# Kernel optimization log

Hardware: AMD Instinct MI355X
Metric: run time of the kernel (lower is better)

## Reference

```python
import jax, jax.numpy as jnp
import numpy as np
import math

NLAT, NLON = 46, 90      # equiangular grid (in_shape == out_shape)
CH = 256                 # channels == kdim == vdim
BATCH = 1

def _cc_weights(n):
    # Clenshaw-Curtis quadrature weights (Waldvogel), nodes cos(k*pi/(n-1)); matches torch-harmonics equiangular grid
    n1 = n - 1
    N = np.arange(1, n1, 2)
    l = len(N)
    m = n1 - l
    v = np.concatenate([2.0 / N / (N - 2), [1.0 / N[-1]], np.zeros(m)])
    v = -v[:-1] - v[-1:0:-1]
    g0 = -np.ones(n1)
    g0[l] += n1
    g0[m] += n1
    g = g0 / (n1 ** 2 - 1 + (n1 % 2))
    w = np.fft.ifft(v + g).real
    return np.concatenate([w, w[:1]])

def _precompute_sparsity():
    # replicates _precompute_neighborhood_sparsity_s2: YZY-rotated north pole indicator within theta_cutoff
    lats = np.linspace(0.0, math.pi, NLAT)               # colatitudes of equiangular grid
    quad = (2.0 * math.pi / NLON) * _cc_weights(NLAT)    # per-latitude quadrature weights
    cutoff = math.pi / (NLAT - 1)                        # default theta_cutoff
    lons = np.linspace(0.0, 2.0 * math.pi, NLON + 1)[:-1]
    rows, cols = [], []
    for t in range(NLAT):
        a = -lats[t]
        beta = lons[None, :]
        gamma = lats[:, None]
        z = -np.cos(beta) * np.sin(a) * np.sin(gamma) + np.cos(a) * np.cos(gamma)
        x = np.cos(a) * np.cos(beta) * np.sin(gamma) + np.cos(gamma) * np.sin(a)
        y = np.sin(beta) * np.sin(gamma)
        nrm = np.sqrt(x * x + y * y + z * z)
        theta = np.arccos(np.clip(z / nrm, -1.0, 1.0))
        ii, jj = np.nonzero(theta <= cutoff)
        rows.append(np.full(ii.shape, t, dtype=np.int64))
        cols.append(ii * NLON + jj)
    row_ids = np.concatenate(rows).astype(np.int32)   # CSR row id per nnz (sorted)
    col_idx = np.concatenate(cols).astype(np.int32)   # flattened input index (at wo=0)
    return row_ids, col_idx, quad.astype(np.float32)

def setup_inputs() -> dict:
    key = jax.random.key(0)
    ks = jax.random.split(key, 9)
    row_ids, col_idx, quad = _precompute_sparsity()
    scale = 0.02  # sane init scale (module uses raw randn; trained weights would be O(this))
    return {
        "qo": jax.random.normal(ks[0], (BATCH, CH, NLAT, NLON), dtype=jnp.float32),
        "ki": jax.random.normal(ks[1], (BATCH, CH, NLAT, NLON), dtype=jnp.float32),
        "vi": jax.random.normal(ks[2], (BATCH, CH, NLAT, NLON), dtype=jnp.float32),
        "q_w": jax.random.normal(ks[3], (CH, CH), dtype=jnp.float32) * scale,
        "k_w": jax.random.normal(ks[4], (CH, CH), dtype=jnp.float32) * scale,
        "v_w": jax.random.normal(ks[5], (CH, CH), dtype=jnp.float32) * scale,
        "q_b": jax.random.normal(ks[6], (CH,), dtype=jnp.float32) * scale,
        "k_b": jax.random.normal(ks[7], (CH,), dtype=jnp.float32) * scale,
        "v_b": jax.random.normal(ks[8], (CH,), dtype=jnp.float32) * scale,
        "quad_w": jnp.asarray(quad),
        "row_ids": jnp.asarray(row_ids),
        "col_idx": jnp.asarray(col_idx),
    }

def reference(qo, ki, vi, q_w, k_w, v_w, q_b, k_b, v_b, quad_w, row_ids, col_idx):
    nlat, nlon = qo.shape[2], qo.shape[3]
    # 1x1 conv projections (F.conv2d with [out,in,1,1] kernels)
    q = jnp.einsum("kc,bchw->bkhw", q_w, qo) + q_b[None, :, None, None]
    k = jnp.einsum("kc,bchw->bkhw", k_w, ki) + k_b[None, :, None, None]
    v = jnp.einsum("vc,bchw->bvhw", v_w, vi) + v_b[None, :, None, None]

    hi = col_idx // nlon                                   # [N] input latitude per nnz
    wi0 = col_idx % nlon                                   # [N] input longitude at wo=0
    wo = jnp.arange(nlon)
    wi = (wi0[:, None] + wo[None, :]) % nlon               # [N, nlon] longitudes rotated by output lon

    kg = k[:, :, hi[:, None], wi]                          # [B, kdim, N, nlon] gathered keys
    qg = q[:, :, row_ids, :]                               # [B, kdim, N, nlon] query of owning output row
    qdotk = jnp.einsum("bcnw,bcnw->nbw", qg, kg)           # [N, B, nlon]

    # quadrature-weighted softmax over each output point's neighborhood (segment = output latitude row)
    seg_max = jax.ops.segment_max(qdotk, row_ids, num_segments=nlat, indices_are_sorted=True)
    seg_max = jax.lax.stop_gradient(seg_max)               # max shift cancels exactly in the ratio
    alpha = jnp.exp(qdotk - seg_max[row_ids]) * quad_w[hi][:, None, None]   # [N, B, nlon]
    denom = jax.ops.segment_sum(alpha, row_ids, num_segments=nlat, indices_are_sorted=True)  # [nlat, B, nlon]

    vg = jnp.transpose(v[:, :, hi[:, None], wi], (2, 0, 1, 3))   # [N, B, vdim, nlon]
    num = jax.ops.segment_sum(alpha[:, :, None, :] * vg, row_ids, num_segments=nlat, indices_are_sorted=True)
    out = num / denom[:, :, None, :]                       # [nlat, B, vdim, nlon]
    return jnp.transpose(out, (1, 2, 0, 3))                # [B, vdim, nlat, nlon]
```

## Files before the change

kernel.cpp:

```cpp
#include <hip/hip_runtime.h>
#include <math.h>

#define NLAT 46
#define NLON 90
#define CH   256
#define HW   (NLAT*NLON)
#define HWP  4160
#define HWT  64
#define NHT  65
#define XSTR 264

#define HEAVY_PER_XCD 45
#define LIGHT_GROUPS_PER_ROW 23
#define LIGHT_UNITS   (42*LIGHT_GROUPS_PER_ROW)
#define LIGHT_PER_XCD 121
#define SLOTS_PER_XCD (HEAVY_PER_XCD + LIGHT_PER_XCD)

typedef __attribute__((ext_vector_type(8))) short short8;
typedef __attribute__((ext_vector_type(4))) float floatx4;

__device__ __forceinline__ ushort f2bf(float f){
  uint u = __float_as_uint(f);
  u += 0x7fff + ((u >> 16) & 1);
  return (ushort)(u >> 16);
}
__device__ __forceinline__ float bf2fs(short s){
  return __uint_as_float(((uint)(ushort)s) << 16);
}

__device__ __forceinline__ int lower_bound_i(const int* __restrict__ a, int n, int key){
  int lo = 0, hi = n;
  while (lo < hi){ int mid = (lo + hi) >> 1; if (a[mid] < key) lo = mid + 1; else hi = mid; }
  return lo;
}

__global__ __launch_bounds__(256) void fproj_kernel(
    const float* __restrict__ qo, const float* __restrict__ ki, const float* __restrict__ vi,
    const float* __restrict__ qw, const float* __restrict__ kw, const float* __restrict__ vw,
    const float* __restrict__ qb, const float* __restrict__ kb, const float* __restrict__ vb,
    ushort* __restrict__ qP, ushort* __restrict__ kP, ushort* __restrict__ vP)
{
  const float* X; const float* Wf; const float* Bias; ushort* Out;
  if (blockIdx.y == 0){ X = qo; Wf = qw; Bias = qb; Out = qP; }
  else if (blockIdx.y == 1){ X = ki; Wf = kw; Bias = kb; Out = kP; }
  else { X = vi; Wf = vw; Bias = vb; Out = vP; }

  __shared__ ushort Xs[HWT][XSTR];

  const int tid = threadIdx.x;
  const int hw0 = blockIdx.x * HWT;

  {
    int hwL = tid & 63;
    int cb  = tid >> 6;
    int hw  = hw0 + hwL;
    bool ok = hw < HW;
    const float* Xp = X + (size_t)(cb*64)*HW + (ok ? hw : 0);
    #pragma unroll
    for (int gq = 0; gq < 8; gq++){
      short8 pk;
      #pragma unroll
      for (int u = 0; u < 8; u++){
        float f = ok ? Xp[(size_t)(gq*8 + u)*HW] : 0.f;
        pk[u] = (short)f2bf(f);
      }
      *(short8*)(&Xs[hwL][cb*64 + gq*8]) = pk;
    }
  }
  __syncthreads();

  const int lane = tid & 63;
  const int wave = tid >> 6;
  const int lm = lane & 15;
  const int lq = lane >> 4;
  const int kout_w = wave * 64;

  const float* Apf = Wf + (size_t)(kout_w + lm)*CH + lq*8;

  floatx4 acc[4][4];
  #pragma unroll
  for (int i = 0; i < 4; i++)
    #pragma unroll
    for (int j = 0; j < 4; j++) acc[i][j] = (floatx4){0,0,0,0};

  #pragma unroll
  for (int k0 = 0; k0 < 8; k0++){
    short8 a[4], b[4];
    #pragma unroll
    for (int i = 0; i < 4; i++){
      const float* p = Apf + (size_t)i*16*CH + k0*32;
      float4 w0 = *(const float4*)p;
      float4 w1 = *(const float4*)(p + 4);
      a[i][0] = (short)f2bf(w0.x); a[i][1] = (short)f2bf(w0.y);
      a[i][2] = (short)f2bf(w0.z); a[i][3] = (short)f2bf(w0.w);
      a[i][4] = (short)f2bf(w1.x); a[i][5] = (short)f2bf(w1.y);
      a[i][6] = (short)f2bf(w1.z); a[i][7] = (short)f2bf(w1.w);
    }
    #pragma unroll
    for (int j = 0; j < 4; j++)
      b[j] = *(const short8*)(&Xs[j*16 + lm][lq*8 + k0*32]);
    #pragma unroll
    for (int i = 0; i < 4; i++)
      #pragma unroll
      for (int j = 0; j < 4; j++)
        acc[i][j] = __builtin_amdgcn_mfma_f32_16x16x32_bf16(a[i], b[j], acc[i][j], 0, 0, 0);
  }

  #pragma unroll
  for (int i = 0; i < 4; i++){
    int kout = kout_w + i*16 + lq*4;
    float4 bias = *(const float4*)(Bias + kout);
    #pragma unroll
    for (int j = 0; j < 4; j++){
      int hw = hw0 + j*16 + lm;
      if (hw < HW){
        ushort4 o;
        o.x = f2bf(acc[i][j][0] + bias.x);
        o.y = f2bf(acc[i][j][1] + bias.y);
        o.z = f2bf(acc[i][j][2] + bias.z);
        o.w = f2bf(acc[i][j][3] + bias.w);
        *(ushort4*)(Out + (size_t)hw*CH + kout) = o;
      }
    }
  }
}

__device__ __forceinline__ void load_q16(const ushort* __restrict__ qP, int row, int gl, float* qf){
  const ushort* qrow = qP + (size_t)row * CH + gl*16;
  short8 q0 = *(const short8*)(qrow);
  short8 q1 = *(const short8*)(qrow + 8);
  #pragma unroll
  for (int u = 0; u < 8; u++){ qf[u] = bf2fs(q0[u]); qf[8+u] = bf2fs(q1[u]); }
}

__device__ __forceinline__ void visit(
    const ushort* __restrict__ kP, const ushort* __restrict__ vP,
    const uint* s_p, const float* s_qw,
    int n, int wo, int gl, const float* qf, float& den, float* acc)
{
  uint p  = s_p[n];
  int base = (int)(p & 0xffffu);
  int wi0  = (int)(p >> 16);
  int adj  = base + wo - ((wi0 + wo >= NLON) ? NLON : 0);
  size_t off = (size_t)adj * CH + gl*16;
  const short8* kp8 = (const short8*)(kP + off);
  short8 k0 = kp8[0], k1 = kp8[1];
  float s = 0.f;
  #pragma unroll
  for (int u = 0; u < 8; u++){
    s += qf[u]   * bf2fs(k0[u]);
    s += qf[8+u] * bf2fs(k1[u]);
  }
  s += __shfl_xor(s, 1, 64);
  s += __shfl_xor(s, 2, 64);
  s += __shfl_xor(s, 4, 64);
  s += __shfl_xor(s, 8, 64);
  float e = __expf(s) * s_qw[n];
  const short8* vp8 = (const short8*)(vP + off);
  short8 v0 = vp8[0], v1 = vp8[1];
  den += e;
  #pragma unroll
  for (int u = 0; u < 8; u++){
    acc[u]   += e * bf2fs(v0[u]);
    acc[8+u] += e * bf2fs(v1[u]);
  }
}

__global__ __launch_bounds__(256) void attn_kernel(
    const ushort* __restrict__ qP, const ushort* __restrict__ kP, const ushort* __restrict__ vP,
    const float* __restrict__ quad_w, const int* __restrict__ row_ids,
    const int* __restrict__ col_idx, int nnz, float* __restrict__ out)
{
  const int bid  = blockIdx.x;
  const int xcd  = bid & 7;
  const int slot = bid >> 3;

  int t, wo0, heavy;
  if (slot < HEAVY_PER_XCD){
    heavy = 1;
    int hu   = xcd * HEAVY_PER_XCD + slot;
    int hidx = hu / NLON;
    t   = (hidx < 2) ? hidx : 42 + hidx;
    wo0 = hu - hidx * NLON;
  } else {
    heavy = 0;
    int lu = xcd * LIGHT_PER_XCD + (slot - HEAVY_PER_XCD);
    if (lu >= LIGHT_UNITS) return;
    int li = lu / LIGHT_GROUPS_PER_ROW;
    t   = li + 2;
    wo0 = (lu - li * LIGHT_GROUPS_PER_ROW) * 4;
  }

  const int tid  = threadIdx.x;
  const int lane = tid & 63;
  const int wave = tid >> 6;
  const int g    = lane >> 4;
  const int gl   = lane & 15;

  const int start = lower_bound_i(row_ids, nnz, t);
  const int end   = lower_bound_i(row_ids, nnz, t + 1);
  const int nv    = end - start;

  __shared__ uint  s_p[256];
  __shared__ float s_qw[256];
  __shared__ float sden[4];
  __shared__ float sacc[4][CH];

  for (int n = tid; n < nv; n += 256){
    int ci  = col_idx[start + n];
    int hi  = ci / NLON;
    int wi0 = ci - hi * NLON;
    s_p[n]  = ((uint)wi0 << 16) | (uint)(hi * NLON + wi0);
    s_qw[n] = quad_w[hi];
  }
  __syncthreads();

  if (heavy){
    float qf[16];
    load_q16(qP, t * NLON + wo0, gl, qf);
    float den = 0.f;
    float acc[16];
    #pragma unroll
    for (int u = 0; u < 16; u++) acc[u] = 0.f;

    for (int n = wave*4 + g; n < nv; n += 16)
      visit(kP, vP, s_p, s_qw, n, wo0, gl, qf, den, acc);

    #pragma unroll
    for (int u = 0; u < 16; u++){
      acc[u] += __shfl_xor(acc[u], 16, 64);
      acc[u] += __shfl_xor(acc[u], 32, 64);
    }
    den += __shfl_xor(den, 16, 64);
    den += __shfl_xor(den, 32, 64);

    if (lane == 0) sden[wave] = den;
    if (g == 0){
      #pragma unroll
      for (int u = 0; u < 16; u++) sacc[wave][gl*16 + u] = acc[u];
    }
    __syncthreads();

    const float D   = sden[0] + sden[1] + sden[2] + sden[3];
    const float num = sacc[0][tid] + sacc[1][tid] + sacc[2][tid] + sacc[3][tid];
    out[(size_t)tid * HW + t * NLON + wo0] = num / D;
  } else {
    const int wo = wo0 + wave;
    if (wo >= NLON) return;

    float qf[16];
    load_q16(qP, t * NLON + wo, gl, qf);
    float den = 0.f;
    float acc[16];
    #pragma unroll
    for (int u = 0; u < 16; u++) acc[u] = 0.f;

    for (int n = g; n < nv; n += 4)
      visit(kP, vP, s_p, s_qw, n, wo, gl, qf, den, acc);

    #pragma unroll
    for (int u = 0; u < 16; u++){
      acc[u] += __shfl_xor(acc[u], 16, 64);
      acc[u] += __shfl_xor(acc[u], 32, 64);
    }
    den += __shfl_xor(den, 16, 64);
    den += __shfl_xor(den, 32, 64);

    const float invD = 1.0f / den;
    #pragma unroll
    for (int j = 0; j < 4; j++){
      float v01 = (g & 1) ? acc[4 + j]  : acc[j];
      float v23 = (g & 1) ? acc[12 + j] : acc[8 + j];
      float val = (g & 2) ? v23 : v01;
      int c = (gl << 4) + (g << 2) + j;
      out[(size_t)c * HW + t * NLON + wo] = val * invD;
    }
  }
}

extern "C" void kernel_launch(void* const* d_in, const int* in_sizes, int n_in,
                              void* d_out, int out_size, void* d_ws, size_t ws_size,
                              hipStream_t stream)
{
  const float* qo   = (const float*)d_in[0];
  const float* ki   = (const float*)d_in[1];
  const float* vi   = (const float*)d_in[2];
  const float* qw   = (const float*)d_in[3];
  const float* kw   = (const float*)d_in[4];
  const float* vw   = (const float*)d_in[5];
  const float* qb   = (const float*)d_in[6];
  const float* kb   = (const float*)d_in[7];
  const float* vb   = (const float*)d_in[8];
  const float* quad = (const float*)d_in[9];
  const int* row_ids = (const int*)d_in[10];
  const int* col_idx = (const int*)d_in[11];
  const int nnz = in_sizes[10];

  ushort* ws = (ushort*)d_ws;
  const size_t TSZ = (size_t)HWP * CH;
  ushort* qP = ws;  ushort* kP = qP + TSZ;  ushort* vP = kP + TSZ;

  fproj_kernel<<<dim3(NHT, 3), 256, 0, stream>>>(qo, ki, vi, qw, kw, vw, qb, kb, vb, qP, kP, vP);
  attn_kernel<<<dim3(8 * SLOTS_PER_XCD), 256, 0, stream>>>(qP, kP, vP, quad, row_ids, col_idx, nnz, (float*)d_out);
}
```

Measured before the change: 121.5 us.

## Precompute bf16 weights and CSR row starts, halve projection tile width

Adds a prep kernel that converts the three weight matrices to bf16 once and builds a row_starts array from the sorted row ids. The projection kernel then loads bf16 weights directly instead of converting fp32 on every block, and uses 32-wide spatial tiles with twice as many blocks to improve occupancy. The attention kernel drops its two per-block binary searches and reads row_starts instead. The cost is an extra kernel launch and more redundant weight reads across the doubled number of projection blocks.

```diff
diff --git a/kernel.cpp b/kernel.cpp
--- a/kernel.cpp
+++ b/kernel.cpp
@@ -6,8 +6,8 @@
 #define CH   256
 #define HW   (NLAT*NLON)
 #define HWP  4160
-#define HWT  64
-#define NHT  65
+#define HWT  32
+#define NHT  130
 #define XSTR 264
 
 #define HEAVY_PER_XCD 45
@@ -28,22 +28,47 @@
   return __uint_as_float(((uint)(ushort)s) << 16);
 }
 
-__device__ __forceinline__ int lower_bound_i(const int* __restrict__ a, int n, int key){
-  int lo = 0, hi = n;
-  while (lo < hi){ int mid = (lo + hi) >> 1; if (a[mid] < key) lo = mid + 1; else hi = mid; }
-  return lo;
+__global__ __launch_bounds__(256) void prep_kernel(
+    const float* __restrict__ qw, const float* __restrict__ kw, const float* __restrict__ vw,
+    const int* __restrict__ row_ids, int nnz,
+    ushort* __restrict__ wQ, ushort* __restrict__ wK, ushort* __restrict__ wV,
+    int* __restrict__ row_starts)
+{
+  const int tid = threadIdx.x;
+  const int b   = blockIdx.x;
+  if (b < 3){
+    const float* W = (b == 0) ? qw : (b == 1) ? kw : vw;
+    ushort* O      = (b == 0) ? wQ : (b == 1) ? wK : wV;
+    for (int i = tid*8; i < CH*CH; i += 256*8){
+      float4 a = *(const float4*)(W + i);
+      float4 c = *(const float4*)(W + i + 4);
+      short8 pk;
+      pk[0] = (short)f2bf(a.x); pk[1] = (short)f2bf(a.y);
+      pk[2] = (short)f2bf(a.z); pk[3] = (short)f2bf(a.w);
+      pk[4] = (short)f2bf(c.x); pk[5] = (short)f2bf(c.y);
+      pk[6] = (short)f2bf(c.z); pk[7] = (short)f2bf(c.w);
+      *(short8*)(O + i) = pk;
+    }
+  } else {
+    if (tid < NLAT + 1) row_starts[tid] = nnz;
+    __syncthreads();
+    for (int i = tid; i < nnz; i += 256){
+      int r = row_ids[i];
+      if (i == 0 || row_ids[i-1] != r) row_starts[r] = i;
+    }
+  }
 }
 
 __global__ __launch_bounds__(256) void fproj_kernel(
     const float* __restrict__ qo, const float* __restrict__ ki, const float* __restrict__ vi,
-    const float* __restrict__ qw, const float* __restrict__ kw, const float* __restrict__ vw,
+    const ushort* __restrict__ wQ, const ushort* __restrict__ wK, const ushort* __restrict__ wV,
     const float* __restrict__ qb, const float* __restrict__ kb, const float* __restrict__ vb,
     ushort* __restrict__ qP, ushort* __restrict__ kP, ushort* __restrict__ vP)
 {
-  const float* X; const float* Wf; const float* Bias; ushort* Out;
-  if (blockIdx.y == 0){ X = qo; Wf = qw; Bias = qb; Out = qP; }
-  else if (blockIdx.y == 1){ X = ki; Wf = kw; Bias = kb; Out = kP; }
-  else { X = vi; Wf = vw; Bias = vb; Out = vP; }
+  const float* X; const ushort* Wb; const float* Bias; ushort* Out;
+  if (blockIdx.y == 0){ X = qo; Wb = wQ; Bias = qb; Out = qP; }
+  else if (blockIdx.y == 1){ X = ki; Wb = wK; Bias = kb; Out = kP; }
+  else { X = vi; Wb = wV; Bias = vb; Out = vP; }
 
   __shared__ ushort Xs[HWT][XSTR];
 
@@ -51,20 +76,20 @@
   const int hw0 = blockIdx.x * HWT;
 
   {
-    int hwL = tid & 63;
-    int cb  = tid >> 6;
+    int hwL = tid & 31;
+    int cb  = tid >> 5;
     int hw  = hw0 + hwL;
     bool ok = hw < HW;
-    const float* Xp = X + (size_t)(cb*64)*HW + (ok ? hw : 0);
-    #pragma unroll
-    for (int gq = 0; gq < 8; gq++){
+    const float* Xp = X + (size_t)(cb*32)*HW + (ok ? hw : 0);
+    #pragma unroll
+    for (int gq = 0; gq < 4; gq++){
       short8 pk;
       #pragma unroll
       for (int u = 0; u < 8; u++){
         float f = ok ? Xp[(size_t)(gq*8 + u)*HW] : 0.f;
         pk[u] = (short)f2bf(f);
       }
-      *(short8*)(&Xs[hwL][cb*64 + gq*8]) = pk;
+      *(short8*)(&Xs[hwL][cb*32 + gq*8]) = pk;
     }
   }
   __syncthreads();
@@ -75,34 +100,27 @@
   const int lq = lane >> 4;
   const int kout_w = wave * 64;
 
-  const float* Apf = Wf + (size_t)(kout_w + lm)*CH + lq*8;
-
-  floatx4 acc[4][4];
+  const ushort* Apf = Wb + (size_t)(kout_w + lm)*CH + lq*8;
+
+  floatx4 acc[4][2];
   #pragma unroll
   for (int i = 0; i < 4; i++)
     #pragma unroll
-    for (int j = 0; j < 4; j++) acc[i][j] = (floatx4){0,0,0,0};
+    for (int j = 0; j < 2; j++) acc[i][j] = (floatx4){0,0,0,0};
 
   #pragma unroll
   for (int k0 = 0; k0 < 8; k0++){
-    short8 a[4], b[4];
-    #pragma unroll
-    for (int i = 0; i < 4; i++){
-      const float* p = Apf + (size_t)i*16*CH + k0*32;
-      float4 w0 = *(const float4*)p;
-      float4 w1 = *(const float4*)(p + 4);
-      a[i][0] = (short)f2bf(w0.x); a[i][1] = (short)f2bf(w0.y);
-      a[i][2] = (short)f2bf(w0.z); a[i][3] = (short)f2bf(w0.w);
-      a[i][4] = (short)f2bf(w1.x); a[i][5] = (short)f2bf(w1.y);
-      a[i][6] = (short)f2bf(w1.z); a[i][7] = (short)f2bf(w1.w);
-    }
-    #pragma unroll
-    for (int j = 0; j < 4; j++)
+    short8 a[4], b[2];
+    #pragma unroll
+    for (int i = 0; i < 4; i++)
+      a[i] = *(const short8*)(Apf + (size_t)i*16*CH + k0*32);
+    #pragma unroll
+    for (int j = 0; j < 2; j++)
       b[j] = *(const short8*)(&Xs[j*16 + lm][lq*8 + k0*32]);
     #pragma unroll
     for (int i = 0; i < 4; i++)
       #pragma unroll
-      for (int j = 0; j < 4; j++)
+      for (int j = 0; j < 2; j++)
         acc[i][j] = __builtin_amdgcn_mfma_f32_16x16x32_bf16(a[i], b[j], acc[i][j], 0, 0, 0);
   }
 
@@ -111,7 +129,7 @@
     int kout = kout_w + i*16 + lq*4;
     float4 bias = *(const float4*)(Bias + kout);
     #pragma unroll
-    for (int j = 0; j < 4; j++){
+    for (int j = 0; j < 2; j++){
       int hw = hw0 + j*16 + lm;
       if (hw < HW){
         ushort4 o;
@@ -168,8 +186,8 @@
 
 __global__ __launch_bounds__(256) void attn_kernel(
     const ushort* __restrict__ qP, const ushort* __restrict__ kP, const ushort* __restrict__ vP,
-    const float* __restrict__ quad_w, const int* __restrict__ row_ids,
-    const int* __restrict__ col_idx, int nnz, float* __restrict__ out)
+    const float* __restrict__ quad_w, const int* __restrict__ row_starts,
+    const int* __restrict__ col_idx, float* __restrict__ out)
 {
   const int bid  = blockIdx.x;
   const int xcd  = bid & 7;
@@ -197,8 +215,8 @@
   const int g    = lane >> 4;
   const int gl   = lane & 15;
 
-  const int start = lower_bound_i(row_ids, nnz, t);
-  const int end   = lower_bound_i(row_ids, nnz, t + 1);
+  const int start = row_starts[t];
+  const int end   = row_starts[t + 1];
   const int nv    = end - start;
 
   __shared__ uint  s_p[256];
@@ -299,7 +317,12 @@
   ushort* ws = (ushort*)d_ws;
   const size_t TSZ = (size_t)HWP * CH;
   ushort* qP = ws;  ushort* kP = qP + TSZ;  ushort* vP = kP + TSZ;
-
-  fproj_kernel<<<dim3(NHT, 3), 256, 0, stream>>>(qo, ki, vi, qw, kw, vw, qb, kb, vb, qP, kP, vP);
-  attn_kernel<<<dim3(8 * SLOTS_PER_XCD), 256, 0, stream>>>(qP, kP, vP, quad, row_ids, col_idx, nnz, (float*)d_out);
-}
+  ushort* wQ = vP + TSZ;
+  ushort* wK = wQ + (size_t)CH*CH;
+  ushort* wV = wK + (size_t)CH*CH;
+  int* row_starts = (int*)(wV + (size_t)CH*CH);
+
+  prep_kernel<<<dim3(4), 256, 0, stream>>>(qw, kw, vw, row_ids, nnz, wQ, wK, wV, row_starts);
+  fproj_kernel<<<dim3(NHT, 3), 256, 0, stream>>>(qo, ki, vi, wQ, wK, wV, qb, kb, vb, qP, kP, vP);
+  attn_kernel<<<dim3(8 * SLOTS_PER_XCD), 256, 0, stream>>>(qP, kP, vP, quad, row_starts, col_idx, (float*)d_out);
+}
```

Result: no change. 123.8 us (+1.8%).
